# Optimization experiments

Hardware: AMD Instinct MI355X
Metric: run time of the kernel (lower is better)

## Reference

```python
import jax, jax.numpy as jnp
import numpy as np

N = 20000
D = 256      # input_dim
F = 256      # output_dim
K = F // 8   # hypernetwork rank (c=8 in source)


def setup_inputs() -> dict:
    key = jax.random.key(0)
    k1, k2, k3, k4, k5 = jax.random.split(key, 5)
    h = jax.random.normal(k1, (N, D), dtype=jnp.float32)
    adj = jax.random.uniform(k2, (N, N), dtype=jnp.float32)
    # xavier-uniform-like small init for params
    W1 = jax.random.normal(k3, (D, K), dtype=jnp.float32) * 0.05
    W2 = jax.random.normal(k4, (K, D, F), dtype=jnp.float32) * 0.05
    b = jax.random.normal(k5, (K, F), dtype=jnp.float32) * 0.05
    return {"h": h, "adj": adj, "W1": W1, "W2": W2, "b": b}


def reference(h, adj, W1, W2, b):
    # node: per-node code vector [N, K]
    node = h @ W1
    # Original: w = einsum('nd,dcf->ncf', node, W2); x = einsum('nc,ncf->nf', h, w)
    # Algebraically identical but avoids the huge [N, D, F] intermediate by
    # contracting the input-dim axis first: [N,K,F] instead of [N,D,F].
    hw = jnp.einsum('nc,kcf->nkf', h, W2)      # [N, K, F]
    x = jnp.einsum('nk,nkf->nf', node, hw)     # [N, F]
    # graph aggregation
    x = adj @ x                                 # [N, F]
    # per-node bias generated from the node code
    x = x + node @ b                            # [N, F]
    return jax.nn.relu(x)
```

## Files before the change

### kernel.cpp

```cpp
#include <hip/hip_runtime.h>
#include <hip/hip_bf16.h>

#define Nn 20000
#define Dd 256
#define Ff 256
#define Kc 32
#define NP2 20096

typedef __attribute__((ext_vector_type(8))) short short8;
typedef __attribute__((ext_vector_type(4))) short short4_t;
typedef __attribute__((ext_vector_type(4))) float float4_t;

static __device__ __forceinline__ short f2bf(float x) {
    union { float f; unsigned u; } v; v.f = x;
    unsigned r = v.u + 0x7FFFu + ((v.u >> 16) & 1u);
    return (short)(r >> 16);
}
static __device__ __forceinline__ short4_t cvt4(float4_t v) {
    short4_t r; r[0] = f2bf(v[0]); r[1] = f2bf(v[1]); r[2] = f2bf(v[2]); r[3] = f2bf(v[3]);
    return r;
}
static __device__ __forceinline__ unsigned cvtpk(float a, float b) {
    unsigned r;
    asm("v_cvt_pk_bf16_f32 %0, %1, %2" : "=v"(r) : "v"(a), "v"(b));
    return r;
}
static __device__ __forceinline__ void glds16(const float* g, float* l) {
    __builtin_amdgcn_global_load_lds(
        (const __attribute__((address_space(1))) unsigned int*)g,
        (__attribute__((address_space(3))) unsigned int*)l,
        16, 0, 0);
}

__global__ __launch_bounds__(256) void k_node(const float* __restrict__ h,
                                              const float* __restrict__ W1,
                                              float* __restrict__ node) {
    int t = blockIdx.x * 256 + threadIdx.x;
    int n = t >> 5, k = t & 31;
    if (n >= Nn) return;
    const float4_t* hr = (const float4_t*)(h + (size_t)n * Dd);
    float s = 0.f;
    #pragma unroll 8
    for (int d4 = 0; d4 < 64; ++d4) {
        float4_t hv = hr[d4];
        #pragma unroll
        for (int j = 0; j < 4; ++j) s += hv[j] * W1[(d4 * 4 + j) * Kc + k];
    }
    node[n * Kc + k] = s;
}

__global__ __launch_bounds__(256) void k_bias(const float* __restrict__ node,
                                              const float* __restrict__ bb,
                                              float* __restrict__ out) {
    int n = blockIdx.x, f = threadIdx.x;
    const float* nr = node + (size_t)n * Kc;
    float s = 0.f;
    #pragma unroll
    for (int k = 0; k < Kc; ++k) s += nr[k] * bb[k * Ff + f];
    out[(size_t)n * Ff + f] = s;
}

__global__ __launch_bounds__(256) void k_packW2(const float* __restrict__ W2,
                                                short* __restrict__ P) {
    int t = blockIdx.x * 256 + threadIdx.x;
    int lane = t & 63;
    int cf = (t >> 6) & 15;
    int dc = (t >> 10) & 7;
    int kk = t >> 13;
    int col = cf * 16 + (lane & 15);
    int d0  = dc * 32 + (lane >> 4) * 8;
    const float* src = W2 + ((size_t)(kk * Dd + d0)) * Ff + col;
    short8 v;
    #pragma unroll
    for (int j = 0; j < 8; ++j) v[j] = f2bf(src[(size_t)j * Ff]);
    *(short8*)(P + (size_t)t * 8) = v;
}

__global__ __launch_bounds__(256, 2) void k_xpre(const float* __restrict__ h,
                                                 const float* __restrict__ node,
                                                 const short* __restrict__ P,
                                                 short* __restrict__ xpre_t) {
    __shared__ short hlds[64 * 264];
    __shared__ float ntl[32 * 64];
    int t = threadIdx.x;
    int n0 = blockIdx.x * 64;

    #pragma unroll
    for (int i = 0; i < 16; ++i) {
        int c = t + i * 256;
        int row = c >> 6, cc = c & 63;
        int n = n0 + row; if (n > Nn - 1) n = Nn - 1;
        float4_t v = *(const float4_t*)(h + (size_t)n * Dd + cc * 4);
        *(short4_t*)&hlds[row * 264 + cc * 4] = cvt4(v);
    }
    #pragma unroll
    for (int i = 0; i < 8; ++i) {
        int idx = t + i * 256;
        int nl = idx >> 5, k = idx & 31;
        int n = n0 + nl; if (n > Nn - 1) n = Nn - 1;
        ntl[k * 64 + nl] = node[(size_t)n * Kc + k];
    }
    __syncthreads();

    int lane = t & 63, w = t >> 6;
    int arow = lane & 15;
    int asel = (lane >> 4) * 8;
    float4_t acc[4][4];
    #pragma unroll
    for (int a = 0; a < 4; ++a)
        #pragma unroll
        for (int b2 = 0; b2 < 4; ++b2) acc[a][b2] = (float4_t){0.f, 0.f, 0.f, 0.f};

    for (int kk = 0; kk < 32; ++kk) {
        float4_t T[4][4];
        #pragma unroll
        for (int a = 0; a < 4; ++a)
            #pragma unroll
            for (int b2 = 0; b2 < 4; ++b2) T[a][b2] = (float4_t){0.f, 0.f, 0.f, 0.f};
        #pragma unroll
        for (int dc = 0; dc < 8; ++dc) {
            short8 af[4], bfr[4];
            #pragma unroll
            for (int rf = 0; rf < 4; ++rf)
                af[rf] = *(const short8*)&hlds[(rf * 16 + arow) * 264 + dc * 32 + asel];
            #pragma unroll
            for (int cf = 0; cf < 4; ++cf)
                bfr[cf] = *(const short8*)(P + ((size_t)(((kk * 8 + dc) * 16 + w * 4 + cf) * 64 + lane)) * 8);
            #pragma unroll
            for (int rf = 0; rf < 4; ++rf)
                #pragma unroll
                for (int cf = 0; cf < 4; ++cf)
                    T[rf][cf] = __builtin_amdgcn_mfma_f32_16x16x32_bf16(af[rf], bfr[cf], T[rf][cf], 0, 0, 0);
        }
        #pragma unroll
        for (int rf = 0; rf < 4; ++rf) {
            float4_t sc = *(const float4_t*)&ntl[kk * 64 + rf * 16 + (lane >> 4) * 4];
            #pragma unroll
            for (int cf = 0; cf < 4; ++cf)
                #pragma unroll
                for (int r = 0; r < 4; ++r)
                    acc[rf][cf][r] += sc[r] * T[rf][cf][r];
        }
    }

    #pragma unroll
    for (int rf = 0; rf < 4; ++rf) {
        int nl = rf * 16 + (lane >> 4) * 4;
        #pragma unroll
        for (int cf = 0; cf < 4; ++cf) {
            int f = w * 64 + cf * 16 + (lane & 15);
            #pragma unroll
            for (int r = 0; r < 4; ++r) {
                int n = n0 + nl + r;
                if (n < Nn)       xpre_t[(size_t)f * NP2 + n] = f2bf(acc[rf][cf][r]);
                else if (n < NP2) xpre_t[(size_t)f * NP2 + n] = 0;
            }
        }
    }
}

__global__ __launch_bounds__(512, 4) void k_aggr(const float* __restrict__ adj,
                                                 const short* __restrict__ xpre_t,
                                                 float* __restrict__ out) {
    __shared__ float lds0[4096], lds1[4096], lds2[4096];

    const int t = threadIdx.x;
    const int lane = t & 63, w = t >> 6;
    const int bid = blockIdx.x;
    const int split = bid >= 313;
    const int m0 = (split ? bid - 313 : bid) * 64;
    const int k0 = split ? 9984 : 0;
    const int ns = split ? 157 : 156;

    long rowbase[2]; int colp[2];
    #pragma unroll
    for (int i = 0; i < 2; ++i) {
        int d = (w * 2 + i) * 256 + lane * 4;
        int row = d >> 6, col = d & 63;
        int r = m0 + row; if (r > Nn - 1) r = Nn - 1;
        rowbase[i] = (long)r * Nn;
        colp[i] = col ^ ((row & 7) << 2);
    }
    const short* bp0 = xpre_t + (long)(w * 32 + (lane & 15)) * NP2 + k0 + (lane >> 4) * 8;
    const short* bp1 = bp0 + 16L * NP2;

    float4_t acc[4][2];
    #pragma unroll
    for (int rf = 0; rf < 4; ++rf) {
        acc[rf][0] = (float4_t){0.f, 0.f, 0.f, 0.f};
        acc[rf][1] = (float4_t){0.f, 0.f, 0.f, 0.f};
    }
    short8 B0[2][2], B1[2][2];

    float* pR = lds0; float* pM = lds1; float* pW = lds2;
    int s = 0;

#define LOADB(Bn_, off_) do { _Pragma("unroll") for (int dc = 0; dc < 2; ++dc) { \
        Bn_[dc][0] = *(const short8*)(bp0 + (off_) + dc * 32); \
        Bn_[dc][1] = *(const short8*)(bp1 + (off_) + dc * 32); } } while (0)

#define STEP(Bc_, Bn_) do { \
        LOADB(Bn_, (long)(s + 1) * 64); \
        asm volatile("s_waitcnt vmcnt(6) lgkmcnt(0)" ::: "memory"); \
        __builtin_amdgcn_s_barrier(); \
        __builtin_amdgcn_sched_barrier(0); \
        _Pragma("unroll") for (int dc = 0; dc < 2; ++dc) { \
            _Pragma("unroll") for (int rf = 0; rf < 4; ++rf) { \
                const int rl = rf * 16 + (lane & 15); \
                const int sw = (rl & 7) << 2; \
                const int c0 = dc * 32 + (lane >> 4) * 8; \
                float4_t lo = *(const float4_t*)&pR[rl * 64 + ((c0    ) ^ sw)]; \
                float4_t hi = *(const float4_t*)&pR[rl * 64 + ((c0 + 4) ^ sw)]; \
                union { short8 s8; unsigned u[4]; } af; \
                af.u[0] = cvtpk(lo[0], lo[1]); af.u[1] = cvtpk(lo[2], lo[3]); \
                af.u[2] = cvtpk(hi[0], hi[1]); af.u[3] = cvtpk(hi[2], hi[3]); \
                acc[rf][0] = __builtin_amdgcn_mfma_f32_16x16x32_bf16(af.s8, Bc_[dc][0], acc[rf][0], 0, 0, 0); \
                acc[rf][1] = __builtin_amdgcn_mfma_f32_16x16x32_bf16(af.s8, Bc_[dc][1], acc[rf][1], 0, 0, 0); } } \
        { int gc0 = k0 + (s + 2) * 64 + colp[0]; if (gc0 > Nn - 4) gc0 = Nn - 4; \
          int gc1 = k0 + (s + 2) * 64 + colp[1]; if (gc1 > Nn - 4) gc1 = Nn - 4; \
          glds16(adj + rowbase[0] + gc0, pW + (w * 2 + 0) * 256); \
          glds16(adj + rowbase[1] + gc1, pW + (w * 2 + 1) * 256); } \
        { float* tp_ = pR; pR = pM; pM = pW; pW = tp_; } \
        ++s; } while (0)

    glds16(adj + rowbase[0] + k0 + colp[0], pR + (w * 2 + 0) * 256);
    glds16(adj + rowbase[1] + k0 + colp[1], pR + (w * 2 + 1) * 256);
    asm volatile("" ::: "memory");
    LOADB(B0, 0L);
    asm volatile("" ::: "memory");
    glds16(adj + rowbase[0] + k0 + 64 + colp[0], pM + (w * 2 + 0) * 256);
    glds16(adj + rowbase[1] + k0 + 64 + colp[1], pM + (w * 2 + 1) * 256);
    asm volatile("" ::: "memory");

    #pragma unroll 1
    for (int p = 0; p < (ns >> 1); ++p) {
        STEP(B0, B1);
        STEP(B1, B0);
    }
    if (ns & 1) STEP(B0, B1);

    #pragma unroll
    for (int rf = 0; rf < 4; ++rf) {
        #pragma unroll
        for (int cf = 0; cf < 2; ++cf) {
            const int fl = w * 32 + cf * 16 + (lane & 15);
            #pragma unroll
            for (int q = 0; q < 4; ++q) {
                int n = m0 + rf * 16 + (lane >> 4) * 4 + q;
                if (n < Nn) atomicAdd(out + (size_t)n * Ff + fl, acc[rf][cf][q]);
            }
        }
    }
#undef LOADB
#undef STEP
}

__global__ __launch_bounds__(256) void k_final(float* __restrict__ out) {
    int i = blockIdx.x * 256 + threadIdx.x;
    float4_t* o = (float4_t*)out;
    #pragma unroll
    for (int j = 0; j < 2; ++j) {
        int idx = i + j * 640000;
        float4_t v = o[idx];
        #pragma unroll
        for (int q = 0; q < 4; ++q) v[q] = v[q] > 0.f ? v[q] : 0.f;
        o[idx] = v;
    }
}

extern "C" void kernel_launch(void* const* d_in, const int* in_sizes, int n_in,
                              void* d_out, int out_size, void* d_ws, size_t ws_size,
                              hipStream_t stream) {
    const float* h   = (const float*)d_in[0];
    const float* adj = (const float*)d_in[1];
    const float* W1  = (const float*)d_in[2];
    const float* W2  = (const float*)d_in[3];
    const float* b   = (const float*)d_in[4];
    float* out = (float*)d_out;

    char* ws = (char*)d_ws;
    float* node   = (float*)ws;
    short* P      = (short*)(ws + 2560000);
    short* xpre_t = (short*)(ws + 2560000 + 4194304);

    k_node  <<<2500, 256, 0, stream>>>(h, W1, node);
    k_bias  <<<Nn,   256, 0, stream>>>(node, b, out);
    k_packW2<<<1024, 256, 0, stream>>>(W2, P);
    k_xpre  <<<314,  256, 0, stream>>>(h, node, P, xpre_t);
    k_aggr  <<<626,  512, 0, stream>>>(adj, xpre_t, out);
    k_final <<<2500, 256, 0, stream>>>(out);
}
```

Before: 1.014 ms.

## Retile adjacency GEMM to 256-row blocks with register-staged bf16 LDS A tiles

The aggregation kernel moves from 64-row tiles with two K splits to 256-row by 256-column tiles using 1024-thread blocks and 13 K splits. Adjacency tiles are now loaded into registers, converted to bf16 once, and written to a double-buffered swizzled LDS buffer, replacing the direct global-to-LDS fp32 loads that were converted at every MFMA read. The goal is to reuse each bf16 B fragment across four times as many rows and to halve LDS traffic. In exchange it uses one block per CU with higher register pressure and more atomic partial-sum adds, and the padded xpre length shrinks to 20032.

```diff
diff --git a/kernel.cpp b/kernel.cpp
--- a/kernel.cpp
+++ b/kernel.cpp
@@ -5,7 +5,9 @@
 #define Dd 256
 #define Ff 256
 #define Kc 32
-#define NP2 20096
+#define NP2 20032
+#define NSPLIT 13
+#define NMT 79
 
 typedef __attribute__((ext_vector_type(8))) short short8;
 typedef __attribute__((ext_vector_type(4))) short short4_t;
@@ -24,12 +26,6 @@
     unsigned r;
     asm("v_cvt_pk_bf16_f32 %0, %1, %2" : "=v"(r) : "v"(a), "v"(b));
     return r;
-}
-static __device__ __forceinline__ void glds16(const float* g, float* l) {
-    __builtin_amdgcn_global_load_lds(
-        (const __attribute__((address_space(1))) unsigned int*)g,
-        (__attribute__((address_space(3))) unsigned int*)l,
-        16, 0, 0);
 }
 
 __global__ __launch_bounds__(256) void k_node(const float* __restrict__ h,
@@ -159,99 +155,100 @@
     }
 }
 
-__global__ __launch_bounds__(512, 4) void k_aggr(const float* __restrict__ adj,
-                                                 const short* __restrict__ xpre_t,
-                                                 float* __restrict__ out) {
-    __shared__ float lds0[4096], lds1[4096], lds2[4096];
+__global__ __launch_bounds__(1024, 1) void k_aggr(const float* __restrict__ adj,
+                                                  const short* __restrict__ xpre_t,
+                                                  float* __restrict__ out) {
+    __shared__ short albuf[2][16384];
 
     const int t = threadIdx.x;
     const int lane = t & 63, w = t >> 6;
+    const int wm = w >> 2, wn = w & 3;
     const int bid = blockIdx.x;
-    const int split = bid >= 313;
-    const int m0 = (split ? bid - 313 : bid) * 64;
-    const int k0 = split ? 9984 : 0;
-    const int ns = split ? 157 : 156;
-
-    long rowbase[2]; int colp[2];
-    #pragma unroll
-    for (int i = 0; i < 2; ++i) {
-        int d = (w * 2 + i) * 256 + lane * 4;
-        int row = d >> 6, col = d & 63;
-        int r = m0 + row; if (r > Nn - 1) r = Nn - 1;
+    const int mt = bid % NMT, split = bid / NMT;
+    const int m0 = mt * 256;
+    const int s_lo = (split == 0) ? 0 : 25 + (split - 1) * 24;
+    const int ns   = (split == 0) ? 25 : 24;
+
+    const int kg4 = (t & 15) * 4;
+    long rowbase[4];
+    #pragma unroll
+    for (int i = 0; i < 4; ++i) {
+        int r = m0 + (t >> 4) + 64 * i; if (r > Nn - 1) r = Nn - 1;
         rowbase[i] = (long)r * Nn;
-        colp[i] = col ^ ((row & 7) << 2);
-    }
-    const short* bp0 = xpre_t + (long)(w * 32 + (lane & 15)) * NP2 + k0 + (lane >> 4) * 8;
-    const short* bp1 = bp0 + 16L * NP2;
-
-    float4_t acc[4][2];
-    #pragma unroll
-    for (int rf = 0; rf < 4; ++rf) {
-        acc[rf][0] = (float4_t){0.f, 0.f, 0.f, 0.f};
-        acc[rf][1] = (float4_t){0.f, 0.f, 0.f, 0.f};
-    }
-    short8 B0[2][2], B1[2][2];
-
-    float* pR = lds0; float* pM = lds1; float* pW = lds2;
-    int s = 0;
-
-#define LOADB(Bn_, off_) do { _Pragma("unroll") for (int dc = 0; dc < 2; ++dc) { \
-        Bn_[dc][0] = *(const short8*)(bp0 + (off_) + dc * 32); \
-        Bn_[dc][1] = *(const short8*)(bp1 + (off_) + dc * 32); } } while (0)
-
-#define STEP(Bc_, Bn_) do { \
-        LOADB(Bn_, (long)(s + 1) * 64); \
-        asm volatile("s_waitcnt vmcnt(6) lgkmcnt(0)" ::: "memory"); \
+    }
+    const short* bp[4];
+    #pragma unroll
+    for (int cf = 0; cf < 4; ++cf)
+        bp[cf] = xpre_t + (long)(wn * 64 + cf * 16 + (lane & 15)) * NP2 + (lane >> 4) * 8;
+
+    float4_t acc[4][4];
+    #pragma unroll
+    for (int rf = 0; rf < 4; ++rf)
+        #pragma unroll
+        for (int cf = 0; cf < 4; ++cf) acc[rf][cf] = (float4_t){0.f, 0.f, 0.f, 0.f};
+
+    float4_t A0[4], A1[4];
+    short8 BA[4][2], BB[4][2];
+
+#define ISSUEA(Ad, s_) do { int ko = (s_) * 64 + kg4; if (ko > Nn - 4) ko = Nn - 4; \
+        _Pragma("unroll") for (int i = 0; i < 4; ++i) \
+            Ad[i] = *(const float4_t*)(adj + rowbase[i] + ko); } while (0)
+
+#define ISSUEB(Bd, s_) do { int sc_ = (s_) > 312 ? 312 : (s_); long off = (long)sc_ * 64; \
+        _Pragma("unroll") for (int cf = 0; cf < 4; ++cf) { \
+            Bd[cf][0] = *(const short8*)(bp[cf] + off); \
+            Bd[cf][1] = *(const short8*)(bp[cf] + off + 32); } } while (0)
+
+#define WRA(As, p_) do { _Pragma("unroll") for (int i = 0; i < 4; ++i) { \
+        int r = (t >> 4) + 64 * i; \
+        int idx = (r * 64 + kg4) ^ ((r & 7) << 3); \
+        union { short4_t s4; unsigned u[2]; } uu; \
+        uu.u[0] = cvtpk(As[i][0], As[i][1]); uu.u[1] = cvtpk(As[i][2], As[i][3]); \
+        *(short4_t*)&albuf[p_][idx] = uu.s4; } } while (0)
+
+#define COMP(Bc, p_) do { _Pragma("unroll") for (int dc = 0; dc < 2; ++dc) \
+        _Pragma("unroll") for (int rf = 0; rf < 4; ++rf) { \
+            int r = wm * 64 + rf * 16 + (lane & 15); \
+            int c = dc * 32 + (lane >> 4) * 8; \
+            short8 af = *(const short8*)&albuf[p_][(r * 64 + c) ^ ((r & 7) << 3)]; \
+            _Pragma("unroll") for (int cf = 0; cf < 4; ++cf) \
+                acc[rf][cf] = __builtin_amdgcn_mfma_f32_16x16x32_bf16(af, Bc[cf][dc], acc[rf][cf], 0, 0, 0); } } while (0)
+
+#define STEP(Ac, An, Bc, Bn, p_, ls_) do { \
+        ISSUEA(An, s_lo + (ls_) + 1); \
+        ISSUEB(Bn, s_lo + (ls_) + 1); \
+        WRA(Ac, p_); \
+        asm volatile("s_waitcnt lgkmcnt(0)" ::: "memory"); \
         __builtin_amdgcn_s_barrier(); \
-        __builtin_amdgcn_sched_barrier(0); \
-        _Pragma("unroll") for (int dc = 0; dc < 2; ++dc) { \
-            _Pragma("unroll") for (int rf = 0; rf < 4; ++rf) { \
-                const int rl = rf * 16 + (lane & 15); \
-                const int sw = (rl & 7) << 2; \
-                const int c0 = dc * 32 + (lane >> 4) * 8; \
-                float4_t lo = *(const float4_t*)&pR[rl * 64 + ((c0    ) ^ sw)]; \
-                float4_t hi = *(const float4_t*)&pR[rl * 64 + ((c0 + 4) ^ sw)]; \
-                union { short8 s8; unsigned u[4]; } af; \
-                af.u[0] = cvtpk(lo[0], lo[1]); af.u[1] = cvtpk(lo[2], lo[3]); \
-                af.u[2] = cvtpk(hi[0], hi[1]); af.u[3] = cvtpk(hi[2], hi[3]); \
-                acc[rf][0] = __builtin_amdgcn_mfma_f32_16x16x32_bf16(af.s8, Bc_[dc][0], acc[rf][0], 0, 0, 0); \
-                acc[rf][1] = __builtin_amdgcn_mfma_f32_16x16x32_bf16(af.s8, Bc_[dc][1], acc[rf][1], 0, 0, 0); } } \
-        { int gc0 = k0 + (s + 2) * 64 + colp[0]; if (gc0 > Nn - 4) gc0 = Nn - 4; \
-          int gc1 = k0 + (s + 2) * 64 + colp[1]; if (gc1 > Nn - 4) gc1 = Nn - 4; \
-          glds16(adj + rowbase[0] + gc0, pW + (w * 2 + 0) * 256); \
-          glds16(adj + rowbase[1] + gc1, pW + (w * 2 + 1) * 256); } \
-        { float* tp_ = pR; pR = pM; pM = pW; pW = tp_; } \
-        ++s; } while (0)
-
-    glds16(adj + rowbase[0] + k0 + colp[0], pR + (w * 2 + 0) * 256);
-    glds16(adj + rowbase[1] + k0 + colp[1], pR + (w * 2 + 1) * 256);
-    asm volatile("" ::: "memory");
-    LOADB(B0, 0L);
-    asm volatile("" ::: "memory");
-    glds16(adj + rowbase[0] + k0 + 64 + colp[0], pM + (w * 2 + 0) * 256);
-    glds16(adj + rowbase[1] + k0 + 64 + colp[1], pM + (w * 2 + 1) * 256);
-    asm volatile("" ::: "memory");
+        COMP(Bc, p_); } while (0)
+
+    ISSUEA(A0, s_lo);
+    ISSUEB(BA, s_lo);
 
     #pragma unroll 1
     for (int p = 0; p < (ns >> 1); ++p) {
-        STEP(B0, B1);
-        STEP(B1, B0);
-    }
-    if (ns & 1) STEP(B0, B1);
+        const int ls = 2 * p;
+        STEP(A0, A1, BA, BB, 0, ls);
+        STEP(A1, A0, BB, BA, 1, ls + 1);
+    }
+    if (ns & 1) STEP(A0, A1, BA, BB, 0, ns - 1);
 
     #pragma unroll
     for (int rf = 0; rf < 4; ++rf) {
         #pragma unroll
-        for (int cf = 0; cf < 2; ++cf) {
-            const int fl = w * 32 + cf * 16 + (lane & 15);
+        for (int cf = 0; cf < 4; ++cf) {
+            const int fl = wn * 64 + cf * 16 + (lane & 15);
             #pragma unroll
             for (int q = 0; q < 4; ++q) {
-                int n = m0 + rf * 16 + (lane >> 4) * 4 + q;
+                int n = m0 + wm * 64 + rf * 16 + (lane >> 4) * 4 + q;
                 if (n < Nn) atomicAdd(out + (size_t)n * Ff + fl, acc[rf][cf][q]);
             }
         }
     }
-#undef LOADB
+#undef ISSUEA
+#undef ISSUEB
+#undef WRA
+#undef COMP
 #undef STEP
 }
 
@@ -286,7 +283,7 @@
     k_node  <<<2500, 256, 0, stream>>>(h, W1, node);
     k_bias  <<<Nn,   256, 0, stream>>>(node, b, out);
     k_packW2<<<1024, 256, 0, stream>>>(W2, P);
-    k_xpre  <<<314,  256, 0, stream>>>(h, node, P, xpre_t);
-    k_aggr  <<<626,  512, 0, stream>>>(adj, xpre_t, out);
+    k_xpre  <<<313,  256, 0, stream>>>(h, node, P, xpre_t);
+    k_aggr  <<<NMT * NSPLIT, 1024, 0, stream>>>(adj, xpre_t, out);
     k_final <<<2500, 256, 0, stream>>>(out);
 }
```

After: 2.777 ms. 174% more time.
